# Performance work log

Hardware: AMD Instinct MI355X
Metric: run time of the kernel (lower is better)

Reference implementation:

```python
import jax, jax.numpy as jnp
import numpy as np

N_NODES = 50000
IN_CH = 128
HID = 32
HEADS = 4
OUT_CH = 32
N_EDGES = 1600000
NEG_SLOPE = 0.2


def _gatv2(x, src, dst, Wl, bl, Wr, br, att, bias, H, C):
    """GATv2Conv (PyG semantics, add_self_loops already applied to src/dst).
    x: [N, F_in]; src/dst: [E]; Wl/Wr: [F_in, H*C]; att: [H, C]; bias: [H*C].
    Returns [N, H*C] (concat heads)."""
    N = x.shape[0]
    xl = (x @ Wl + bl).reshape(N, H, C)  # source-side transform
    xr = (x @ Wr + br).reshape(N, H, C)  # target-side transform
    e = jax.nn.leaky_relu(xl[src] + xr[dst], NEG_SLOPE)  # [E, H, C]
    logits = jnp.einsum('ehc,hc->eh', e, att)  # [E, H]
    # softmax over incoming edges of each target node (stable)
    m = jax.ops.segment_max(logits, dst, num_segments=N)[dst]
    p = jnp.exp(logits - m)
    denom = jax.ops.segment_sum(p, dst, num_segments=N)[dst]
    alpha = p / denom  # [E, H]
    out = jax.ops.segment_sum(alpha[:, :, None] * xl[src], dst, num_segments=N)
    return out.reshape(N, H * C) + bias


def setup_inputs() -> dict:
    key = jax.random.key(0)
    ks = jax.random.split(key, 16)
    s1 = 1.0 / np.sqrt(IN_CH)
    s2 = 1.0 / np.sqrt(HID * HEADS)
    inp = {
        'x': jax.random.normal(ks[0], (N_NODES, IN_CH), jnp.float32),
        'edge_index': jax.random.randint(ks[1], (2, N_EDGES), 0, N_NODES, jnp.int64 if jax.config.read('jax_enable_x64') else jnp.int32).astype(jnp.int32),
        # layer 1: in -> HID per head, HEADS heads
        'Wl1': jax.random.normal(ks[2], (IN_CH, HEADS * HID), jnp.float32) * s1,
        'bl1': jnp.zeros((HEADS * HID,), jnp.float32),
        'Wr1': jax.random.normal(ks[3], (IN_CH, HEADS * HID), jnp.float32) * s1,
        'br1': jnp.zeros((HEADS * HID,), jnp.float32),
        'att1': jax.random.normal(ks[4], (HEADS, HID), jnp.float32) * s1,
        'b1': jnp.zeros((HEADS * HID,), jnp.float32),
        # mu head: HID*HEADS -> OUT_CH, 1 head
        'Wl_mu': jax.random.normal(ks[5], (HEADS * HID, OUT_CH), jnp.float32) * s2,
        'bl_mu': jnp.zeros((OUT_CH,), jnp.float32),
        'Wr_mu': jax.random.normal(ks[6], (HEADS * HID, OUT_CH), jnp.float32) * s2,
        'br_mu': jnp.zeros((OUT_CH,), jnp.float32),
        'att_mu': jax.random.normal(ks[7], (1, OUT_CH), jnp.float32) * s2,
        'b_mu': jnp.zeros((OUT_CH,), jnp.float32),
        # logvar head
        'Wl_lv': jax.random.normal(ks[8], (HEADS * HID, OUT_CH), jnp.float32) * s2,
        'bl_lv': jnp.zeros((OUT_CH,), jnp.float32),
        'Wr_lv': jax.random.normal(ks[9], (HEADS * HID, OUT_CH), jnp.float32) * s2,
        'br_lv': jnp.zeros((OUT_CH,), jnp.float32),
        'att_lv': jax.random.normal(ks[10], (1, OUT_CH), jnp.float32) * s2,
        'b_lv': jnp.zeros((OUT_CH,), jnp.float32),
    }
    return inp


def reference(x, edge_index, Wl1, bl1, Wr1, br1, att1, b1,
              Wl_mu, bl_mu, Wr_mu, br_mu, att_mu, b_mu,
              Wl_lv, bl_lv, Wr_lv, br_lv, att_lv, b_lv):
    N = x.shape[0]
    loops = jnp.arange(N, dtype=edge_index.dtype)
    src = jnp.concatenate([edge_index[0], loops])  # add_self_loops=True
    dst = jnp.concatenate([edge_index[1], loops])
    h = jax.nn.relu(_gatv2(x, src, dst, Wl1, bl1, Wr1, br1, att1, b1, HEADS, HID))
    mu = _gatv2(h, src, dst, Wl_mu, bl_mu, Wr_mu, br_mu, att_mu, b_mu, 1, OUT_CH)
    logvar = _gatv2(h, src, dst, Wl_lv, bl_lv, Wr_lv, br_lv, att_lv, b_lv, 1, OUT_CH)
    return (mu, logvar)
```

## Files before the change

kernel.cpp:

```cpp
#include <hip/hip_runtime.h>
#include <hip/hip_fp16.h>

#define NNODES 50000
#define EORIG  1600000
#define ETOT   (EORIG + NNODES)
#define NEG 0.2f
#define BSH 7
#define NBUCK ((NNODES + 127) >> BSH)
#define BCAP 5120
#define NRT (NNODES / 16)
#define EPB 4096
#define LOG2E 1.44269504f

typedef _Float16 v2h __attribute__((ext_vector_type(2)));
typedef _Float16 v8h __attribute__((ext_vector_type(8)));
typedef float    v4f __attribute__((ext_vector_type(4)));

__device__ __forceinline__ float hdot2v(v2h a, v2h b, float c) {
#if __has_builtin(__builtin_amdgcn_fdot2)
    return __builtin_amdgcn_fdot2(a, b, c, false);
#else
    return c + (float)a.x * (float)b.x + (float)a.y * (float)b.y;
#endif
}

__device__ __forceinline__ float fexp2(float t) {
#if __has_builtin(__builtin_amdgcn_exp2f)
    return __builtin_amdgcn_exp2f(t);
#else
    return exp2f(t);
#endif
}

__global__ __launch_bounds__(256) void wcvt_kernel(
    const float* __restrict__ Wl, const float* __restrict__ Wr,
    const float* __restrict__ Wlmu, const float* __restrict__ Wllv,
    const float* __restrict__ Wrmu, const float* __restrict__ Wrlv,
    __half* __restrict__ WT, __half* __restrict__ WT2, int* __restrict__ bcur)
{
    int id = blockIdx.x * 256 + threadIdx.x;
    if (id < NBUCK) bcur[id] = 0;
    if (id < 32768) {
        int k = id >> 8, c = id & 255;
        float v = (c < 128) ? Wl[k * 128 + c] : Wr[k * 128 + (c - 128)];
        WT[c * 128 + k] = __float2half(v);
    } else if (id < 49152) {
        int loc = id - 32768;
        int k = loc >> 7, c = loc & 127;
        int sel = c >> 5, cc = c & 31;
        const float* W = sel == 0 ? Wlmu : sel == 1 ? Wllv : sel == 2 ? Wrmu : Wrlv;
        WT2[c * 128 + k] = __float2half(W[k * 32 + cc]);
    }
}

__global__ __launch_bounds__(256) void lin1_kernel(
    const float* __restrict__ x, const __half* __restrict__ WT,
    const float* __restrict__ bl, const float* __restrict__ br,
    __half* __restrict__ xl16, __half* __restrict__ xr16)
{
    int rt = (blockIdx.x * 256 + threadIdx.x) >> 6;
    if (rt >= NRT) return;
    int l  = threadIdx.x & 63;
    int lr = l & 15, lg = l >> 4;
    int row = rt * 16 + lr;

    v8h a[4];
    const float4* xrow = reinterpret_cast<const float4*>(x + (size_t)row * 128);
    #pragma unroll
    for (int ks = 0; ks < 4; ++ks) {
        float4 f0 = xrow[ks * 8 + lg * 2];
        float4 f1 = xrow[ks * 8 + lg * 2 + 1];
        v8h t;
        t[0]=(_Float16)f0.x; t[1]=(_Float16)f0.y; t[2]=(_Float16)f0.z; t[3]=(_Float16)f0.w;
        t[4]=(_Float16)f1.x; t[5]=(_Float16)f1.y; t[6]=(_Float16)f1.z; t[7]=(_Float16)f1.w;
        a[ks] = t;
    }

    const uint4* wt4 = reinterpret_cast<const uint4*>(WT);
    #pragma unroll 4
    for (int ct = 0; ct < 16; ++ct) {
        int c = ct * 16 + lr;
        v4f acc = {0.f, 0.f, 0.f, 0.f};
        #pragma unroll
        for (int ks = 0; ks < 4; ++ks) {
            union { uint4 u; v8h h; } B;
            B.u = wt4[(size_t)c * 16 + ks * 4 + lg];
            acc = __builtin_amdgcn_mfma_f32_16x16x32_f16(a[ks], B.h, acc, 0, 0, 0);
        }
        float bb = (c < 128) ? bl[c] : br[c - 128];
        #pragma unroll
        for (int j = 0; j < 4; ++j) {
            int orow = rt * 16 + lg * 4 + j;
            __half hv = __float2half(acc[j] + bb);
            if (c < 128) xl16[(size_t)orow * 128 + c] = hv;
            else         xr16[(size_t)orow * 128 + (c - 128)] = hv;
        }
    }
}

__global__ __launch_bounds__(256) void lin2_kernel(
    const __half* __restrict__ h16, const __half* __restrict__ WT2,
    const float* __restrict__ blmu, const float* __restrict__ bllv,
    const float* __restrict__ brmu, const float* __restrict__ brlv,
    __half* __restrict__ xi16, __half* __restrict__ xrI16)
{
    int rt = (blockIdx.x * 256 + threadIdx.x) >> 6;
    if (rt >= NRT) return;
    int l  = threadIdx.x & 63;
    int lr = l & 15, lg = l >> 4;
    int row = rt * 16 + lr;

    v8h a[4];
    const uint4* hrow = reinterpret_cast<const uint4*>(h16 + (size_t)row * 128);
    #pragma unroll
    for (int ks = 0; ks < 4; ++ks) {
        union { uint4 u; v8h h; } A;
        A.u = hrow[ks * 4 + lg];
        a[ks] = A.h;
    }

    const uint4* wt4 = reinterpret_cast<const uint4*>(WT2);
    #pragma unroll 4
    for (int ct = 0; ct < 8; ++ct) {
        int c = ct * 16 + lr;
        v4f acc = {0.f, 0.f, 0.f, 0.f};
        #pragma unroll
        for (int ks = 0; ks < 4; ++ks) {
            union { uint4 u; v8h h; } B;
            B.u = wt4[(size_t)c * 16 + ks * 4 + lg];
            acc = __builtin_amdgcn_mfma_f32_16x16x32_f16(a[ks], B.h, acc, 0, 0, 0);
        }
        int sel = c >> 5, cc = c & 31;
        const float* bp = sel == 0 ? blmu : sel == 1 ? bllv : sel == 2 ? brmu : brlv;
        float bb = bp[cc];
        #pragma unroll
        for (int j = 0; j < 4; ++j) {
            int orow = rt * 16 + lg * 4 + j;
            __half hv = __float2half(acc[j] + bb);
            if (c < 64) xi16 [(size_t)orow * 64 + c]      = hv;
            else        xrI16[(size_t)orow * 64 + (c-64)] = hv;
        }
    }
}

__global__ __launch_bounds__(256) void part_kernel(
    const int* __restrict__ src, const int* __restrict__ dst,
    int* __restrict__ bcur, unsigned int* __restrict__ pairs)
{
    __shared__ int cnt[NBUCK];
    __shared__ int gbase[NBUCK];
    const int e0 = blockIdx.x * EPB;

    for (int i = threadIdx.x; i < NBUCK; i += 256) cnt[i] = 0;
    __syncthreads();

    for (int i = threadIdx.x; i < EPB; i += 256) {
        int e = e0 + i;
        if (e >= ETOT) break;
        int d = (e < EORIG) ? dst[e] : e - EORIG;
        atomicAdd(&cnt[d >> BSH], 1);
    }
    __syncthreads();

    for (int b = threadIdx.x; b < NBUCK; b += 256) {
        int c = cnt[b];
        gbase[b] = c ? (b * BCAP + atomicAdd(&bcur[b], c)) : 0;
        cnt[b] = 0;
    }
    __syncthreads();

    for (int i = threadIdx.x; i < EPB; i += 256) {
        int e = e0 + i;
        if (e >= ETOT) break;
        int s, d;
        if (e < EORIG) { s = src[e]; d = dst[e]; }
        else           { s = d = e - EORIG; }
        int b = d >> BSH;
        int slot = atomicAdd(&cnt[b], 1);
        pairs[gbase[b] + slot] = (unsigned)s | ((unsigned)(d & 127) << 16);
    }
}

__global__ __launch_bounds__(256) void csrfill_kernel(
    const unsigned int* __restrict__ pairs, const int* __restrict__ bcur,
    int2* __restrict__ begend, unsigned short* __restrict__ csr)
{
    __shared__ int cnt[128];
    __shared__ int lofs[128];
    __shared__ int scnt[128];
    const int b = blockIdx.x, n0 = b << BSH;
    const int nn = min(128, NNODES - n0);
    const int pbase = b * BCAP;
    const int pend = pbase + bcur[b];
    const int t = threadIdx.x;

    if (t < 128) { cnt[t] = 0; scnt[t] = 0; }
    __syncthreads();
    for (int i = pbase + t; i < pend; i += 256)
        atomicAdd(&cnt[pairs[i] >> 16], 1);
    __syncthreads();

    if (t < 128) lofs[t] = cnt[t];
    __syncthreads();
    for (int off = 1; off < 128; off <<= 1) {
        int v = (t < 128 && t >= off) ? lofs[t - off] : 0;
        __syncthreads();
        if (t < 128) lofs[t] += v;
        __syncthreads();
    }
    if (t < 128) lofs[t] = pbase + lofs[t] - cnt[t];
    __syncthreads();

    if (t < nn) begend[n0 + t] = make_int2(lofs[t], lofs[t] + cnt[t]);

    for (int i = pbase + t; i < pend; i += 256) {
        unsigned pr = pairs[i];
        int l = pr >> 16;
        int slot = atomicAdd(&scnt[l], 1);
        csr[lofs[l] + slot] = (unsigned short)(pr & 0xFFFFu);
    }
}

__global__ __launch_bounds__(256) void gat_gather1(
    const __half* __restrict__ xl16, const __half* __restrict__ xr16,
    const float* __restrict__ att, const float* __restrict__ bias,
    const int2* __restrict__ begend, const unsigned short* __restrict__ csr,
    __half* __restrict__ h16)
{
    int d = (blockIdx.x * 256 + threadIdx.x) >> 6;
    if (d >= NNODES) return;
    int lane = threadIdx.x & 63;
    int quarter = lane >> 4;
    int q = lane & 15;
    int qo = quarter * 4;

    v2h xrh[4], ath[4];
    {
        union { uint4 u; v2h v[4]; } R;
        R.u = reinterpret_cast<const uint4*>(xr16)[(size_t)d * 16 + q];
        #pragma unroll
        for (int j = 0; j < 4; ++j) xrh[j] = R.v[j];
        const float4* t4 = reinterpret_cast<const float4*>(att) + q * 2;
        float4 a = t4[0], b = t4[1];
        ath[0] = (v2h){(_Float16)(a.x*LOG2E), (_Float16)(a.y*LOG2E)};
        ath[1] = (v2h){(_Float16)(a.z*LOG2E), (_Float16)(a.w*LOG2E)};
        ath[2] = (v2h){(_Float16)(b.x*LOG2E), (_Float16)(b.y*LOG2E)};
        ath[3] = (v2h){(_Float16)(b.z*LOG2E), (_Float16)(b.w*LOG2E)};
    }
    const v2h neg2 = (v2h){(_Float16)NEG, (_Float16)NEG};

    int2 be = begend[d];
    int beg = be.x, end = be.y;
    int nI = (end - beg + 15) >> 4;
    const uint4* xlu = reinterpret_cast<const uint4*>(xl16);

    float den = 0.f;
    float acc[8] = {0.f,0.f,0.f,0.f,0.f,0.f,0.f,0.f};

    auto compute = [&](uint4 U, bool val) {
        union { uint4 u; v2h v[4]; } X; X.u = U;
        float t = 0.f;
        #pragma unroll
        for (int j = 0; j < 4; ++j) {
            v2h s = X.v[j] + xrh[j];
            v2h l = __builtin_elementwise_max(s, s * neg2);
            t = hdot2v(l, ath[j], t);
        }
        t += __shfl_xor(t, 1, 64);
        t += __shfl_xor(t, 2, 64);
        float p = val ? fexp2(t) : 0.f;
        den += p;
        #pragma unroll
        for (int j = 0; j < 4; ++j) {
            acc[2*j]   += p * (float)X.v[j].x;
            acc[2*j+1] += p * (float)X.v[j].y;
        }
    };

    int  iA[4], iB[4];
    bool vA[4], vB[4];
    uint4 rA[4];

    #pragma unroll
    for (int k = 0; k < 4; ++k) {
        int s = beg + qo + k;
        vA[k] = s < end;
        iA[k] = csr[vA[k] ? s : end - 1];
    }
    #pragma unroll
    for (int k = 0; k < 4; ++k) rA[k] = xlu[(size_t)iA[k] * 16 + q];
    #pragma unroll
    for (int k = 0; k < 4; ++k) {
        int s = beg + 16 + qo + k;
        vB[k] = s < end;
        iB[k] = csr[vB[k] ? s : end - 1];
    }

    for (int it = 0; it < nI; ++it) {
        int b2 = beg + (it + 2) * 16;
        int  iC[4]; bool vC[4];
        #pragma unroll
        for (int k = 0; k < 4; ++k) {
            int s = b2 + qo + k;
            vC[k] = s < end;
            iC[k] = csr[vC[k] ? s : end - 1];
        }
        uint4 rB[4];
        #pragma unroll
        for (int k = 0; k < 4; ++k) rB[k] = xlu[(size_t)iB[k] * 16 + q];
        #pragma unroll
        for (int k = 0; k < 4; ++k) compute(rA[k], vA[k]);
        #pragma unroll
        for (int k = 0; k < 4; ++k) {
            rA[k] = rB[k]; vA[k] = vB[k];
            iB[k] = iC[k]; vB[k] = vC[k];
        }
    }

    den += __shfl_xor(den, 16, 64);
    den += __shfl_xor(den, 32, 64);
    #pragma unroll
    for (int j = 0; j < 8; ++j) {
        acc[j] += __shfl_xor(acc[j], 16, 64);
        acc[j] += __shfl_xor(acc[j], 32, 64);
    }

    if (quarter == 0) {
        float r = 1.f / den;
        const float4* bp = reinterpret_cast<const float4*>(bias) + q * 2;
        float4 ba = bp[0], bb = bp[1];
        __half hv[8];
        hv[0] = __float2half(fmaxf(acc[0]*r+ba.x, 0.f));
        hv[1] = __float2half(fmaxf(acc[1]*r+ba.y, 0.f));
        hv[2] = __float2half(fmaxf(acc[2]*r+ba.z, 0.f));
        hv[3] = __float2half(fmaxf(acc[3]*r+ba.w, 0.f));
        hv[4] = __float2half(fmaxf(acc[4]*r+bb.x, 0.f));
        hv[5] = __float2half(fmaxf(acc[5]*r+bb.y, 0.f));
        hv[6] = __float2half(fmaxf(acc[6]*r+bb.z, 0.f));
        hv[7] = __float2half(fmaxf(acc[7]*r+bb.w, 0.f));
        *reinterpret_cast<uint4*>(&h16[(size_t)d * 128 + q * 8]) =
            *reinterpret_cast<uint4*>(hv);
    }
}

__global__ __launch_bounds__(256) void gat_gather2(
    const __half* __restrict__ xi16, const __half* __restrict__ xrI16,
    const float* __restrict__ atmu, const float* __restrict__ atlv,
    const float* __restrict__ bmu,  const float* __restrict__ blv,
    const int2* __restrict__ begend, const unsigned short* __restrict__ csr,
    float* __restrict__ out)
{
    int d = (blockIdx.x * 256 + threadIdx.x) >> 6;
    if (d >= NNODES) return;
    int lane = threadIdx.x & 63;
    int oct = lane >> 3;
    int r   = lane & 7;
    bool lv = r >= 4;
    int cq  = lv ? r - 4 : r;
    int oo = oct * 2;

    v2h xrh[4], ath[4];
    {
        union { uint4 u; v2h v[4]; } R;
        R.u = reinterpret_cast<const uint4*>(xrI16)[(size_t)d * 8 + r];
        #pragma unroll
        for (int j = 0; j < 4; ++j) xrh[j] = R.v[j];
        const float4* t4 = reinterpret_cast<const float4*>(lv ? atlv : atmu) + cq * 2;
        float4 a = t4[0], b = t4[1];
        ath[0] = (v2h){(_Float16)(a.x*LOG2E), (_Float16)(a.y*LOG2E)};
        ath[1] = (v2h){(_Float16)(a.z*LOG2E), (_Float16)(a.w*LOG2E)};
        ath[2] = (v2h){(_Float16)(b.x*LOG2E), (_Float16)(b.y*LOG2E)};
        ath[3] = (v2h){(_Float16)(b.z*LOG2E), (_Float16)(b.w*LOG2E)};
    }
    const v2h neg2 = (v2h){(_Float16)NEG, (_Float16)NEG};

    int2 be = begend[d];
    int beg = be.x, end = be.y;
    int nI = (end - beg + 15) >> 4;
    const uint4* xiu = reinterpret_cast<const uint4*>(xi16);

    float den = 0.f;
    float acc[8] = {0.f,0.f,0.f,0.f,0.f,0.f,0.f,0.f};

    auto compute = [&](uint4 U, bool val) {
        union { uint4 u; v2h v[4]; } X; X.u = U;
        float t = 0.f;
        #pragma unroll
        for (int j = 0; j < 4; ++j) {
            v2h s = X.v[j] + xrh[j];
            v2h l = __builtin_elementwise_max(s, s * neg2);
            t = hdot2v(l, ath[j], t);
        }
        t += __shfl_xor(t, 1, 64);
        t += __shfl_xor(t, 2, 64);
        float p = val ? fexp2(t) : 0.f;
        den += p;
        #pragma unroll
        for (int j = 0; j < 4; ++j) {
            acc[2*j]   += p * (float)X.v[j].x;
            acc[2*j+1] += p * (float)X.v[j].y;
        }
    };

    int  iA[2], iB[2];
    bool vA[2], vB[2];
    uint4 rA[2];

    #pragma unroll
    for (int k = 0; k < 2; ++k) {
        int s = beg + oo + k;
        vA[k] = s < end;
        iA[k] = csr[vA[k] ? s : end - 1];
    }
    #pragma unroll
    for (int k = 0; k < 2; ++k) rA[k] = xiu[(size_t)iA[k] * 8 + r];
    #pragma unroll
    for (int k = 0; k < 2; ++k) {
        int s = beg + 16 + oo + k;
        vB[k] = s < end;
        iB[k] = csr[vB[k] ? s : end - 1];
    }

    for (int it = 0; it < nI; ++it) {
        int b2 = beg + (it + 2) * 16;
        int  iC[2]; bool vC[2];
        #pragma unroll
        for (int k = 0; k < 2; ++k) {
            int s = b2 + oo + k;
            vC[k] = s < end;
            iC[k] = csr[vC[k] ? s : end - 1];
        }
        uint4 rB[2];
        #pragma unroll
        for (int k = 0; k < 2; ++k) rB[k] = xiu[(size_t)iB[k] * 8 + r];
        #pragma unroll
        for (int k = 0; k < 2; ++k) compute(rA[k], vA[k]);
        #pragma unroll
        for (int k = 0; k < 2; ++k) {
            rA[k] = rB[k]; vA[k] = vB[k];
            iB[k] = iC[k]; vB[k] = vC[k];
        }
    }

    den += __shfl_xor(den, 8, 64);
    den += __shfl_xor(den, 16, 64);
    den += __shfl_xor(den, 32, 64);
    #pragma unroll
    for (int j = 0; j < 8; ++j) {
        acc[j] += __shfl_xor(acc[j], 8, 64);
        acc[j] += __shfl_xor(acc[j], 16, 64);
        acc[j] += __shfl_xor(acc[j], 32, 64);
    }

    if (oct == 0) {
        float rr = 1.f / den;
        const float4* bp = reinterpret_cast<const float4*>(lv ? blv : bmu) + cq * 2;
        float4 ba = bp[0], bb = bp[1];
        float4 o1 = make_float4(acc[0]*rr+ba.x, acc[1]*rr+ba.y,
                                acc[2]*rr+ba.z, acc[3]*rr+ba.w);
        float4 o2 = make_float4(acc[4]*rr+bb.x, acc[5]*rr+bb.y,
                                acc[6]*rr+bb.z, acc[7]*rr+bb.w);
        float* base_out = out + (lv ? 1600000 : 0);
        float4* op = reinterpret_cast<float4*>(base_out) + (size_t)d * 8 + cq * 2;
        op[0] = o1; op[1] = o2;
    }
}

extern "C" void kernel_launch(void* const* d_in, const int* in_sizes, int n_in,
                              void* d_out, int out_size, void* d_ws, size_t ws_size,
                              hipStream_t stream) {
    const float* x    = (const float*)d_in[0];
    const int*   ei   = (const int*)d_in[1];
    const float* Wl1  = (const float*)d_in[2];
    const float* bl1  = (const float*)d_in[3];
    const float* Wr1  = (const float*)d_in[4];
    const float* br1  = (const float*)d_in[5];
    const float* att1 = (const float*)d_in[6];
    const float* b1   = (const float*)d_in[7];
    const float* Wlmu = (const float*)d_in[8];
    const float* blmu = (const float*)d_in[9];
    const float* Wrmu = (const float*)d_in[10];
    const float* brmu = (const float*)d_in[11];
    const float* atmu = (const float*)d_in[12];
    const float* bmu  = (const float*)d_in[13];
    const float* Wllv = (const float*)d_in[14];
    const float* bllv = (const float*)d_in[15];
    const float* Wrlv = (const float*)d_in[16];
    const float* brlv = (const float*)d_in[17];
    const float* atlv = (const float*)d_in[18];
    const float* blv  = (const float*)d_in[19];

    float* out = (float*)d_out;
    float* ws  = (float*)d_ws;

    __half* xl16 = (__half*)ws;
    __half* xr16 = (__half*)(ws + 3200000);
    __half* h16  = (__half*)(ws + 6400000);
    __half* WT   = (__half*)(ws + 9600000);
    __half* WT2  = (__half*)(ws + 9620000);

    __half* xi16  = (__half*)ws;
    __half* xrI16 = (__half*)(ws + 1600000);

    int* ip = (int*)(ws + 10000000);
    unsigned int*   pairs  = (unsigned int*)ip;
    int*            bcur   = ip + 2001920;
    int2*           begend = (int2*)(ip + 2002312);
    unsigned short* csr    = (unsigned short*)(ip + 2102312);

    const int* srcp = ei;
    const int* dstp = ei + EORIG;

    const int NBE = (ETOT + EPB - 1) / EPB;

    wcvt_kernel<<<192, 256, 0, stream>>>(Wl1, Wr1, Wlmu, Wllv, Wrmu, Wrlv, WT, WT2, bcur);

    part_kernel<<<NBE, 256, 0, stream>>>(srcp, dstp, bcur, pairs);
    csrfill_kernel<<<NBUCK, 256, 0, stream>>>(pairs, bcur, begend, csr);

    lin1_kernel<<<(NRT + 3) / 4, 256, 0, stream>>>(x, WT, bl1, br1, xl16, xr16);

    gat_gather1<<<(NNODES * 64 + 255) / 256, 256, 0, stream>>>(
        xl16, xr16, att1, b1, begend, csr, h16);

    lin2_kernel<<<(NRT + 3) / 4, 256, 0, stream>>>(
        h16, WT2, blmu, bllv, brmu, brlv, xi16, xrI16);

    gat_gather2<<<(NNODES * 64 + 255) / 256, 256, 0, stream>>>(
        xi16, xrI16, atmu, atlv, bmu, blv, begend, csr, out);
}
```

Before: 198.5 us.

## Store node features head-major and gather one head per wavefront

Node feature buffers move from row-major [N, H*C] to head-major [H, N, 32], and both gather kernels now assign one head of one destination node per wavefront. Eight edges are processed per iteration using 8-byte loads, and blocks are arranged so that wavefronts working on the same head run close together. The goal is a smaller per-head gather footprint, so the source-feature table for that head stays in L2 and the random gathers touch fewer cache lines. The weight conversion is merged into the partition kernel with a memset replacing the in-kernel counter reset. This removes a launch, but the CSR indices and edge lists are now read once per head and each wavefront does less work per load.

```diff
diff --git a/kernel.cpp b/kernel.cpp
--- a/kernel.cpp
+++ b/kernel.cpp
@@ -10,6 +10,7 @@
 #define BCAP 5120
 #define NRT (NNODES / 16)
 #define EPB 4096
+#define NBE ((ETOT + EPB - 1) / EPB)
 #define LOG2E 1.44269504f
 
 typedef _Float16 v2h __attribute__((ext_vector_type(2)));
@@ -32,31 +33,109 @@
 #endif
 }
 
-__global__ __launch_bounds__(256) void wcvt_kernel(
+__global__ __launch_bounds__(256) void prep_kernel(
+    const int* __restrict__ src, const int* __restrict__ dst,
+    int* __restrict__ bcur, unsigned int* __restrict__ pairs,
     const float* __restrict__ Wl, const float* __restrict__ Wr,
     const float* __restrict__ Wlmu, const float* __restrict__ Wllv,
     const float* __restrict__ Wrmu, const float* __restrict__ Wrlv,
-    __half* __restrict__ WT, __half* __restrict__ WT2, int* __restrict__ bcur)
-{
-    int id = blockIdx.x * 256 + threadIdx.x;
-    if (id < NBUCK) bcur[id] = 0;
-    if (id < 32768) {
-        int k = id >> 8, c = id & 255;
-        float v = (c < 128) ? Wl[k * 128 + c] : Wr[k * 128 + (c - 128)];
-        WT[c * 128 + k] = __float2half(v);
-    } else if (id < 49152) {
-        int loc = id - 32768;
-        int k = loc >> 7, c = loc & 127;
-        int sel = c >> 5, cc = c & 31;
-        const float* W = sel == 0 ? Wlmu : sel == 1 ? Wllv : sel == 2 ? Wrmu : Wrlv;
-        WT2[c * 128 + k] = __float2half(W[k * 32 + cc]);
+    __half* __restrict__ WT, __half* __restrict__ WT2)
+{
+    if (blockIdx.x >= NBE) {
+        int id = (blockIdx.x - NBE) * 256 + threadIdx.x;
+        if (id < 32768) {
+            int k = id >> 8, c = id & 255;
+            float v = (c < 128) ? Wl[k * 128 + c] : Wr[k * 128 + (c - 128)];
+            WT[c * 128 + k] = __float2half(v);
+        } else if (id < 49152) {
+            int loc = id - 32768;
+            int k = loc >> 7, c = loc & 127;
+            int sel = c >> 5, cc = c & 31;
+            const float* W = sel == 0 ? Wlmu : sel == 1 ? Wllv : sel == 2 ? Wrmu : Wrlv;
+            WT2[c * 128 + k] = __float2half(W[k * 32 + cc]);
+        }
+        return;
+    }
+
+    __shared__ int cnt[NBUCK];
+    __shared__ int gbase[NBUCK];
+    const int e0 = blockIdx.x * EPB;
+
+    for (int i = threadIdx.x; i < NBUCK; i += 256) cnt[i] = 0;
+    __syncthreads();
+
+    for (int i = threadIdx.x; i < EPB; i += 256) {
+        int e = e0 + i;
+        if (e >= ETOT) break;
+        int d = (e < EORIG) ? dst[e] : e - EORIG;
+        atomicAdd(&cnt[d >> BSH], 1);
+    }
+    __syncthreads();
+
+    for (int b = threadIdx.x; b < NBUCK; b += 256) {
+        int c = cnt[b];
+        gbase[b] = c ? (b * BCAP + atomicAdd(&bcur[b], c)) : 0;
+        cnt[b] = 0;
+    }
+    __syncthreads();
+
+    for (int i = threadIdx.x; i < EPB; i += 256) {
+        int e = e0 + i;
+        if (e >= ETOT) break;
+        int s, d;
+        if (e < EORIG) { s = src[e]; d = dst[e]; }
+        else           { s = d = e - EORIG; }
+        int b = d >> BSH;
+        int slot = atomicAdd(&cnt[b], 1);
+        pairs[gbase[b] + slot] = (unsigned)s | ((unsigned)(d & 127) << 16);
+    }
+}
+
+__global__ __launch_bounds__(256) void csrfill_kernel(
+    const unsigned int* __restrict__ pairs, const int* __restrict__ bcur,
+    int2* __restrict__ begend, unsigned short* __restrict__ csr)
+{
+    __shared__ int cnt[128];
+    __shared__ int lofs[128];
+    __shared__ int scnt[128];
+    const int b = blockIdx.x, n0 = b << BSH;
+    const int nn = min(128, NNODES - n0);
+    const int pbase = b * BCAP;
+    const int pend = pbase + bcur[b];
+    const int t = threadIdx.x;
+
+    if (t < 128) { cnt[t] = 0; scnt[t] = 0; }
+    __syncthreads();
+    for (int i = pbase + t; i < pend; i += 256)
+        atomicAdd(&cnt[pairs[i] >> 16], 1);
+    __syncthreads();
+
+    int myc = (t < 128) ? cnt[t] : 0;
+    if (t < 128) lofs[t] = myc;
+    __syncthreads();
+    for (int off = 1; off < 128; off <<= 1) {
+        int v = (t < 128 && t >= off) ? lofs[t - off] : 0;
+        __syncthreads();
+        if (t < 128) lofs[t] += v;
+        __syncthreads();
+    }
+    if (t < 128) lofs[t] = pbase + lofs[t] - myc;
+    __syncthreads();
+
+    if (t < nn) begend[n0 + t] = make_int2(lofs[t], lofs[t] + myc);
+
+    for (int i = pbase + t; i < pend; i += 256) {
+        unsigned pr = pairs[i];
+        int l = pr >> 16;
+        int slot = atomicAdd(&scnt[l], 1);
+        csr[lofs[l] + slot] = (unsigned short)(pr & 0xFFFFu);
     }
 }
 
 __global__ __launch_bounds__(256) void lin1_kernel(
     const float* __restrict__ x, const __half* __restrict__ WT,
     const float* __restrict__ bl, const float* __restrict__ br,
-    __half* __restrict__ xl16, __half* __restrict__ xr16)
+    __half* __restrict__ xlh, __half* __restrict__ xrh)
 {
     int rt = (blockIdx.x * 256 + threadIdx.x) >> 6;
     if (rt >= NRT) return;
@@ -88,21 +167,22 @@
             acc = __builtin_amdgcn_mfma_f32_16x16x32_f16(a[ks], B.h, acc, 0, 0, 0);
         }
         float bb = (c < 128) ? bl[c] : br[c - 128];
+        int c2 = (c < 128) ? c : c - 128;
+        __half* dstp = (c < 128) ? xlh : xrh;
+        int hh = c2 >> 5, cc = c2 & 31;
         #pragma unroll
         for (int j = 0; j < 4; ++j) {
             int orow = rt * 16 + lg * 4 + j;
-            __half hv = __float2half(acc[j] + bb);
-            if (c < 128) xl16[(size_t)orow * 128 + c] = hv;
-            else         xr16[(size_t)orow * 128 + (c - 128)] = hv;
+            dstp[((size_t)hh * NNODES + orow) * 32 + cc] = __float2half(acc[j] + bb);
         }
     }
 }
 
 __global__ __launch_bounds__(256) void lin2_kernel(
-    const __half* __restrict__ h16, const __half* __restrict__ WT2,
+    const __half* __restrict__ h16h, const __half* __restrict__ WT2,
     const float* __restrict__ blmu, const float* __restrict__ bllv,
     const float* __restrict__ brmu, const float* __restrict__ brlv,
-    __half* __restrict__ xi16, __half* __restrict__ xrI16)
+    __half* __restrict__ xi, __half* __restrict__ xr2)
 {
     int rt = (blockIdx.x * 256 + threadIdx.x) >> 6;
     if (rt >= NRT) return;
@@ -111,11 +191,11 @@
     int row = rt * 16 + lr;
 
     v8h a[4];
-    const uint4* hrow = reinterpret_cast<const uint4*>(h16 + (size_t)row * 128);
     #pragma unroll
     for (int ks = 0; ks < 4; ++ks) {
         union { uint4 u; v8h h; } A;
-        A.u = hrow[ks * 4 + lg];
+        A.u = *reinterpret_cast<const uint4*>(
+            h16h + ((size_t)ks * NNODES + row) * 32 + lg * 8);
         a[ks] = A.h;
     }
 
@@ -133,336 +213,202 @@
         int sel = c >> 5, cc = c & 31;
         const float* bp = sel == 0 ? blmu : sel == 1 ? bllv : sel == 2 ? brmu : brlv;
         float bb = bp[cc];
+        __half* dstp = (sel < 2) ? (xi + (size_t)sel * NNODES * 32)
+                                 : (xr2 + (size_t)(sel - 2) * NNODES * 32);
         #pragma unroll
         for (int j = 0; j < 4; ++j) {
             int orow = rt * 16 + lg * 4 + j;
-            __half hv = __float2half(acc[j] + bb);
-            if (c < 64) xi16 [(size_t)orow * 64 + c]      = hv;
-            else        xrI16[(size_t)orow * 64 + (c-64)] = hv;
+            dstp[(size_t)orow * 32 + cc] = __float2half(acc[j] + bb);
         }
     }
 }
 
-__global__ __launch_bounds__(256) void part_kernel(
-    const int* __restrict__ src, const int* __restrict__ dst,
-    int* __restrict__ bcur, unsigned int* __restrict__ pairs)
-{
-    __shared__ int cnt[NBUCK];
-    __shared__ int gbase[NBUCK];
-    const int e0 = blockIdx.x * EPB;
-
-    for (int i = threadIdx.x; i < NBUCK; i += 256) cnt[i] = 0;
-    __syncthreads();
-
-    for (int i = threadIdx.x; i < EPB; i += 256) {
-        int e = e0 + i;
-        if (e >= ETOT) break;
-        int d = (e < EORIG) ? dst[e] : e - EORIG;
-        atomicAdd(&cnt[d >> BSH], 1);
-    }
-    __syncthreads();
-
-    for (int b = threadIdx.x; b < NBUCK; b += 256) {
-        int c = cnt[b];
-        gbase[b] = c ? (b * BCAP + atomicAdd(&bcur[b], c)) : 0;
-        cnt[b] = 0;
-    }
-    __syncthreads();
-
-    for (int i = threadIdx.x; i < EPB; i += 256) {
-        int e = e0 + i;
-        if (e >= ETOT) break;
-        int s, d;
-        if (e < EORIG) { s = src[e]; d = dst[e]; }
-        else           { s = d = e - EORIG; }
-        int b = d >> BSH;
-        int slot = atomicAdd(&cnt[b], 1);
-        pairs[gbase[b] + slot] = (unsigned)s | ((unsigned)(d & 127) << 16);
-    }
-}
-
-__global__ __launch_bounds__(256) void csrfill_kernel(
-    const unsigned int* __restrict__ pairs, const int* __restrict__ bcur,
-    int2* __restrict__ begend, unsigned short* __restrict__ csr)
-{
-    __shared__ int cnt[128];
-    __shared__ int lofs[128];
-    __shared__ int scnt[128];
-    const int b = blockIdx.x, n0 = b << BSH;
-    const int nn = min(128, NNODES - n0);
-    const int pbase = b * BCAP;
-    const int pend = pbase + bcur[b];
-    const int t = threadIdx.x;
-
-    if (t < 128) { cnt[t] = 0; scnt[t] = 0; }
-    __syncthreads();
-    for (int i = pbase + t; i < pend; i += 256)
-        atomicAdd(&cnt[pairs[i] >> 16], 1);
-    __syncthreads();
-
-    if (t < 128) lofs[t] = cnt[t];
-    __syncthreads();
-    for (int off = 1; off < 128; off <<= 1) {
-        int v = (t < 128 && t >= off) ? lofs[t - off] : 0;
-        __syncthreads();
-        if (t < 128) lofs[t] += v;
-        __syncthreads();
-    }
-    if (t < 128) lofs[t] = pbase + lofs[t] - cnt[t];
-    __syncthreads();
-
-    if (t < nn) begend[n0 + t] = make_int2(lofs[t], lofs[t] + cnt[t]);
-
-    for (int i = pbase + t; i < pend; i += 256) {
-        unsigned pr = pairs[i];
-        int l = pr >> 16;
-        int slot = atomicAdd(&scnt[l], 1);
-        csr[lofs[l] + slot] = (unsigned short)(pr & 0xFFFFu);
-    }
-}
-
 __global__ __launch_bounds__(256) void gat_gather1(
-    const __half* __restrict__ xl16, const __half* __restrict__ xr16,
+    const __half* __restrict__ xlh, const __half* __restrict__ xrh,
     const float* __restrict__ att, const float* __restrict__ bias,
     const int2* __restrict__ begend, const unsigned short* __restrict__ csr,
-    __half* __restrict__ h16)
-{
-    int d = (blockIdx.x * 256 + threadIdx.x) >> 6;
+    __half* __restrict__ h16h)
+{
+    int b = blockIdx.x;
+    int s = b & 7;
+    int head = s >> 1;
+    int d = (b >> 3) * 8 + (s & 1) * 4 + (threadIdx.x >> 6);
     if (d >= NNODES) return;
     int lane = threadIdx.x & 63;
-    int quarter = lane >> 4;
-    int q = lane & 15;
-    int qo = quarter * 4;
-
-    v2h xrh[4], ath[4];
+    int g = lane >> 3;
+    int c = lane & 7;
+
+    v2h xrv[2], atv[2];
     {
-        union { uint4 u; v2h v[4]; } R;
-        R.u = reinterpret_cast<const uint4*>(xr16)[(size_t)d * 16 + q];
-        #pragma unroll
-        for (int j = 0; j < 4; ++j) xrh[j] = R.v[j];
-        const float4* t4 = reinterpret_cast<const float4*>(att) + q * 2;
-        float4 a = t4[0], b = t4[1];
-        ath[0] = (v2h){(_Float16)(a.x*LOG2E), (_Float16)(a.y*LOG2E)};
-        ath[1] = (v2h){(_Float16)(a.z*LOG2E), (_Float16)(a.w*LOG2E)};
-        ath[2] = (v2h){(_Float16)(b.x*LOG2E), (_Float16)(b.y*LOG2E)};
-        ath[3] = (v2h){(_Float16)(b.z*LOG2E), (_Float16)(b.w*LOG2E)};
+        union { uint2 u; v2h v[2]; } R;
+        R.u = reinterpret_cast<const uint2*>(xrh + ((size_t)head * NNODES + d) * 32)[c];
+        xrv[0] = R.v[0]; xrv[1] = R.v[1];
+        float4 a = reinterpret_cast<const float4*>(att + head * 32)[c];
+        atv[0] = (v2h){(_Float16)(a.x*LOG2E), (_Float16)(a.y*LOG2E)};
+        atv[1] = (v2h){(_Float16)(a.z*LOG2E), (_Float16)(a.w*LOG2E)};
     }
     const v2h neg2 = (v2h){(_Float16)NEG, (_Float16)NEG};
 
     int2 be = begend[d];
     int beg = be.x, end = be.y;
-    int nI = (end - beg + 15) >> 4;
-    const uint4* xlu = reinterpret_cast<const uint4*>(xl16);
+    int nI = (end - beg + 7) >> 3;
+    const uint2* xlu = reinterpret_cast<const uint2*>(xlh + (size_t)head * NNODES * 32);
 
     float den = 0.f;
-    float acc[8] = {0.f,0.f,0.f,0.f,0.f,0.f,0.f,0.f};
-
-    auto compute = [&](uint4 U, bool val) {
-        union { uint4 u; v2h v[4]; } X; X.u = U;
-        float t = 0.f;
-        #pragma unroll
-        for (int j = 0; j < 4; ++j) {
-            v2h s = X.v[j] + xrh[j];
-            v2h l = __builtin_elementwise_max(s, s * neg2);
-            t = hdot2v(l, ath[j], t);
-        }
+    float acc[4] = {0.f, 0.f, 0.f, 0.f};
+
+    auto compute = [&](uint2 U, bool val) {
+        union { uint2 u; v2h v[2]; } X; X.u = U;
+        v2h s0 = X.v[0] + xrv[0];
+        v2h s1 = X.v[1] + xrv[1];
+        v2h l0 = __builtin_elementwise_max(s0, s0 * neg2);
+        v2h l1 = __builtin_elementwise_max(s1, s1 * neg2);
+        float t = hdot2v(l0, atv[0], 0.f);
+        t = hdot2v(l1, atv[1], t);
         t += __shfl_xor(t, 1, 64);
         t += __shfl_xor(t, 2, 64);
+        t += __shfl_xor(t, 4, 64);
         float p = val ? fexp2(t) : 0.f;
         den += p;
-        #pragma unroll
-        for (int j = 0; j < 4; ++j) {
-            acc[2*j]   += p * (float)X.v[j].x;
-            acc[2*j+1] += p * (float)X.v[j].y;
-        }
+        acc[0] += p * (float)X.v[0].x;
+        acc[1] += p * (float)X.v[0].y;
+        acc[2] += p * (float)X.v[1].x;
+        acc[3] += p * (float)X.v[1].y;
     };
 
-    int  iA[4], iB[4];
-    bool vA[4], vB[4];
-    uint4 rA[4];
-
-    #pragma unroll
-    for (int k = 0; k < 4; ++k) {
-        int s = beg + qo + k;
-        vA[k] = s < end;
-        iA[k] = csr[vA[k] ? s : end - 1];
-    }
-    #pragma unroll
-    for (int k = 0; k < 4; ++k) rA[k] = xlu[(size_t)iA[k] * 16 + q];
-    #pragma unroll
-    for (int k = 0; k < 4; ++k) {
-        int s = beg + 16 + qo + k;
-        vB[k] = s < end;
-        iB[k] = csr[vB[k] ? s : end - 1];
-    }
+    int sA = beg + g;
+    bool vA = sA < end;
+    int iA = csr[vA ? sA : end - 1];
+    uint2 rA = xlu[(size_t)iA * 8 + c];
+    int sB = beg + 8 + g;
+    bool vB = sB < end;
+    int iB = csr[vB ? sB : end - 1];
 
     for (int it = 0; it < nI; ++it) {
-        int b2 = beg + (it + 2) * 16;
-        int  iC[4]; bool vC[4];
-        #pragma unroll
-        for (int k = 0; k < 4; ++k) {
-            int s = b2 + qo + k;
-            vC[k] = s < end;
-            iC[k] = csr[vC[k] ? s : end - 1];
-        }
-        uint4 rB[4];
-        #pragma unroll
-        for (int k = 0; k < 4; ++k) rB[k] = xlu[(size_t)iB[k] * 16 + q];
-        #pragma unroll
-        for (int k = 0; k < 4; ++k) compute(rA[k], vA[k]);
-        #pragma unroll
-        for (int k = 0; k < 4; ++k) {
-            rA[k] = rB[k]; vA[k] = vB[k];
-            iB[k] = iC[k]; vB[k] = vC[k];
-        }
-    }
-
+        int sC = beg + (it + 2) * 8 + g;
+        bool vC = sC < end;
+        int iC = csr[vC ? sC : end - 1];
+        uint2 rB = xlu[(size_t)iB * 8 + c];
+        compute(rA, vA);
+        rA = rB; vA = vB; iB = iC; vB = vC;
+    }
+
+    den += __shfl_xor(den, 8, 64);
     den += __shfl_xor(den, 16, 64);
     den += __shfl_xor(den, 32, 64);
     #pragma unroll
-    for (int j = 0; j < 8; ++j) {
+    for (int j = 0; j < 4; ++j) {
+        acc[j] += __shfl_xor(acc[j], 8, 64);
         acc[j] += __shfl_xor(acc[j], 16, 64);
         acc[j] += __shfl_xor(acc[j], 32, 64);
     }
 
-    if (quarter == 0) {
+    if (g == 0) {
         float r = 1.f / den;
-        const float4* bp = reinterpret_cast<const float4*>(bias) + q * 2;
-        float4 ba = bp[0], bb = bp[1];
-        __half hv[8];
-        hv[0] = __float2half(fmaxf(acc[0]*r+ba.x, 0.f));
-        hv[1] = __float2half(fmaxf(acc[1]*r+ba.y, 0.f));
-        hv[2] = __float2half(fmaxf(acc[2]*r+ba.z, 0.f));
-        hv[3] = __float2half(fmaxf(acc[3]*r+ba.w, 0.f));
-        hv[4] = __float2half(fmaxf(acc[4]*r+bb.x, 0.f));
-        hv[5] = __float2half(fmaxf(acc[5]*r+bb.y, 0.f));
-        hv[6] = __float2half(fmaxf(acc[6]*r+bb.z, 0.f));
-        hv[7] = __float2half(fmaxf(acc[7]*r+bb.w, 0.f));
-        *reinterpret_cast<uint4*>(&h16[(size_t)d * 128 + q * 8]) =
-            *reinterpret_cast<uint4*>(hv);
+        float4 bb = reinterpret_cast<const float4*>(bias + head * 32)[c];
+        __half hv[4];
+        hv[0] = __float2half(fmaxf(acc[0] * r + bb.x, 0.f));
+        hv[1] = __float2half(fmaxf(acc[1] * r + bb.y, 0.f));
+        hv[2] = __float2half(fmaxf(acc[2] * r + bb.z, 0.f));
+        hv[3] = __float2half(fmaxf(acc[3] * r + bb.w, 0.f));
+        *reinterpret_cast<uint2*>(&h16h[((size_t)head * NNODES + d) * 32 + c * 4]) =
+            *reinterpret_cast<uint2*>(hv);
     }
 }
 
 __global__ __launch_bounds__(256) void gat_gather2(
-    const __half* __restrict__ xi16, const __half* __restrict__ xrI16,
+    const __half* __restrict__ xi, const __half* __restrict__ xr2,
     const float* __restrict__ atmu, const float* __restrict__ atlv,
     const float* __restrict__ bmu,  const float* __restrict__ blv,
     const int2* __restrict__ begend, const unsigned short* __restrict__ csr,
     float* __restrict__ out)
 {
-    int d = (blockIdx.x * 256 + threadIdx.x) >> 6;
+    int b = blockIdx.x;
+    int s = b & 7;
+    int head = s >> 2;
+    int d = (b >> 3) * 16 + (s & 3) * 4 + (threadIdx.x >> 6);
     if (d >= NNODES) return;
     int lane = threadIdx.x & 63;
-    int oct = lane >> 3;
-    int r   = lane & 7;
-    bool lv = r >= 4;
-    int cq  = lv ? r - 4 : r;
-    int oo = oct * 2;
-
-    v2h xrh[4], ath[4];
+    int g = lane >> 3;
+    int c = lane & 7;
+
+    const __half* xip  = xi  + (size_t)head * NNODES * 32;
+    const __half* xrp  = xr2 + (size_t)head * NNODES * 32;
+    const float*  atp  = head ? atlv : atmu;
+    const float*  bp   = head ? blv : bmu;
+
+    v2h xrv[2], atv[2];
     {
-        union { uint4 u; v2h v[4]; } R;
-        R.u = reinterpret_cast<const uint4*>(xrI16)[(size_t)d * 8 + r];
-        #pragma unroll
-        for (int j = 0; j < 4; ++j) xrh[j] = R.v[j];
-        const float4* t4 = reinterpret_cast<const float4*>(lv ? atlv : atmu) + cq * 2;
-        float4 a = t4[0], b = t4[1];
-        ath[0] = (v2h){(_Float16)(a.x*LOG2E), (_Float16)(a.y*LOG2E)};
-        ath[1] = (v2h){(_Float16)(a.z*LOG2E), (_Float16)(a.w*LOG2E)};
-        ath[2] = (v2h){(_Float16)(b.x*LOG2E), (_Float16)(b.y*LOG2E)};
-        ath[3] = (v2h){(_Float16)(b.z*LOG2E), (_Float16)(b.w*LOG2E)};
+        union { uint2 u; v2h v[2]; } R;
+        R.u = reinterpret_cast<const uint2*>(xrp + (size_t)d * 32)[c];
+        xrv[0] = R.v[0]; xrv[1] = R.v[1];
+        float4 a = reinterpret_cast<const float4*>(atp)[c];
+        atv[0] = (v2h){(_Float16)(a.x*LOG2E), (_Float16)(a.y*LOG2E)};
+        atv[1] = (v2h){(_Float16)(a.z*LOG2E), (_Float16)(a.w*LOG2E)};
     }
     const v2h neg2 = (v2h){(_Float16)NEG, (_Float16)NEG};
 
     int2 be = begend[d];
     int beg = be.x, end = be.y;
-    int nI = (end - beg + 15) >> 4;
-    const uint4* xiu = reinterpret_cast<const uint4*>(xi16);
+    int nI = (end - beg + 7) >> 3;
+    const uint2* xiu = reinterpret_cast<const uint2*>(xip);
 
     float den = 0.f;
-    float acc[8] = {0.f,0.f,0.f,0.f,0.f,0.f,0.f,0.f};
-
-    auto compute = [&](uint4 U, bool val) {
-        union { uint4 u; v2h v[4]; } X; X.u = U;
-        float t = 0.f;
-        #pragma unroll
-        for (int j = 0; j < 4; ++j) {
-            v2h s = X.v[j] + xrh[j];
-            v2h l = __builtin_elementwise_max(s, s * neg2);
-            t = hdot2v(l, ath[j], t);
-        }
+    float acc[4] = {0.f, 0.f, 0.f, 0.f};
+
+    auto compute = [&](uint2 U, bool val) {
+        union { uint2 u; v2h v[2]; } X; X.u = U;
+        v2h s0 = X.v[0] + xrv[0];
+        v2h s1 = X.v[1] + xrv[1];
+        v2h l0 = __builtin_elementwise_max(s0, s0 * neg2);
+        v2h l1 = __builtin_elementwise_max(s1, s1 * neg2);
+        float t = hdot2v(l0, atv[0], 0.f);
+        t = hdot2v(l1, atv[1], t);
         t += __shfl_xor(t, 1, 64);
         t += __shfl_xor(t, 2, 64);
+        t += __shfl_xor(t, 4, 64);
         float p = val ? fexp2(t) : 0.f;
         den += p;
-        #pragma unroll
-        for (int j = 0; j < 4; ++j) {
-            acc[2*j]   += p * (float)X.v[j].x;
-            acc[2*j+1] += p * (float)X.v[j].y;
-        }
+        acc[0] += p * (float)X.v[0].x;
+        acc[1] += p * (float)X.v[0].y;
+        acc[2] += p * (float)X.v[1].x;
+        acc[3] += p * (float)X.v[1].y;
     };
 
-    int  iA[2], iB[2];
-    bool vA[2], vB[2];
-    uint4 rA[2];
-
-    #pragma unroll
-    for (int k = 0; k < 2; ++k) {
-        int s = beg + oo + k;
-        vA[k] = s < end;
-        iA[k] = csr[vA[k] ? s : end - 1];
-    }
-    #pragma unroll
-    for (int k = 0; k < 2; ++k) rA[k] = xiu[(size_t)iA[k] * 8 + r];
-    #pragma unroll
-    for (int k = 0; k < 2; ++k) {
-        int s = beg + 16 + oo + k;
-        vB[k] = s < end;
-        iB[k] = csr[vB[k] ? s : end - 1];
-    }
+    int sA = beg + g;
+    bool vA = sA < end;
+    int iA = csr[vA ? sA : end - 1];
+    uint2 rA = xiu[(size_t)iA * 8 + c];
+    int sB = beg + 8 + g;
+    bool vB = sB < end;
+    int iB = csr[vB ? sB : end - 1];
 
     for (int it = 0; it < nI; ++it) {
-        int b2 = beg + (it + 2) * 16;
-        int  iC[2]; bool vC[2];
-        #pragma unroll
-        for (int k = 0; k < 2; ++k) {
-            int s = b2 + oo + k;
-            vC[k] = s < end;
-            iC[k] = csr[vC[k] ? s : end - 1];
-        }
-        uint4 rB[2];
-        #pragma unroll
-        for (int k = 0; k < 2; ++k) rB[k] = xiu[(size_t)iB[k] * 8 + r];
-        #pragma unroll
-        for (int k = 0; k < 2; ++k) compute(rA[k], vA[k]);
-        #pragma unroll
-        for (int k = 0; k < 2; ++k) {
-            rA[k] = rB[k]; vA[k] = vB[k];
-            iB[k] = iC[k]; vB[k] = vC[k];
-        }
+        int sC = beg + (it + 2) * 8 + g;
+        bool vC = sC < end;
+        int iC = csr[vC ? sC : end - 1];
+        uint2 rB = xiu[(size_t)iB * 8 + c];
+        compute(rA, vA);
+        rA = rB; vA = vB; iB = iC; vB = vC;
     }
 
     den += __shfl_xor(den, 8, 64);
     den += __shfl_xor(den, 16, 64);
     den += __shfl_xor(den, 32, 64);
     #pragma unroll
-    for (int j = 0; j < 8; ++j) {
+    for (int j = 0; j < 4; ++j) {
         acc[j] += __shfl_xor(acc[j], 8, 64);
         acc[j] += __shfl_xor(acc[j], 16, 64);
         acc[j] += __shfl_xor(acc[j], 32, 64);
     }
 
-    if (oct == 0) {
-        float rr = 1.f / den;
-        const float4* bp = reinterpret_cast<const float4*>(lv ? blv : bmu) + cq * 2;
-        float4 ba = bp[0], bb = bp[1];
-        float4 o1 = make_float4(acc[0]*rr+ba.x, acc[1]*rr+ba.y,
-                                acc[2]*rr+ba.z, acc[3]*rr+ba.w);
-        float4 o2 = make_float4(acc[4]*rr+bb.x, acc[5]*rr+bb.y,
-                                acc[6]*rr+bb.z, acc[7]*rr+bb.w);
-        float* base_out = out + (lv ? 1600000 : 0);
-        float4* op = reinterpret_cast<float4*>(base_out) + (size_t)d * 8 + cq * 2;
-        op[0] = o1; op[1] = o2;
+    if (g == 0) {
+        float r = 1.f / den;
+        float4 bb = reinterpret_cast<const float4*>(bp)[c];
+        float4 o = make_float4(acc[0]*r+bb.x, acc[1]*r+bb.y,
+                               acc[2]*r+bb.z, acc[3]*r+bb.w);
+        float* base_out = out + (head ? 1600000 : 0);
+        reinterpret_cast<float4*>(base_out + (size_t)d * 32)[c] = o;
     }
 }
 
@@ -493,14 +439,14 @@
     float* out = (float*)d_out;
     float* ws  = (float*)d_ws;
 
-    __half* xl16 = (__half*)ws;
-    __half* xr16 = (__half*)(ws + 3200000);
-    __half* h16  = (__half*)(ws + 6400000);
+    __half* xlh  = (__half*)ws;
+    __half* xrh  = (__half*)(ws + 3200000);
+    __half* h16h = (__half*)(ws + 6400000);
     __half* WT   = (__half*)(ws + 9600000);
     __half* WT2  = (__half*)(ws + 9620000);
 
-    __half* xi16  = (__half*)ws;
-    __half* xrI16 = (__half*)(ws + 1600000);
+    __half* xi  = (__half*)ws;
+    __half* xr2 = (__half*)(ws + 1600000);
 
     int* ip = (int*)(ws + 10000000);
     unsigned int*   pairs  = (unsigned int*)ip;
@@ -511,21 +457,19 @@
     const int* srcp = ei;
     const int* dstp = ei + EORIG;
 
-    const int NBE = (ETOT + EPB - 1) / EPB;
-
-    wcvt_kernel<<<192, 256, 0, stream>>>(Wl1, Wr1, Wlmu, Wllv, Wrmu, Wrlv, WT, WT2, bcur);
-
-    part_kernel<<<NBE, 256, 0, stream>>>(srcp, dstp, bcur, pairs);
+    hipMemsetAsync(bcur, 0, NBUCK * sizeof(int), stream);
+    prep_kernel<<<NBE + 192, 256, 0, stream>>>(
+        srcp, dstp, bcur, pairs, Wl1, Wr1, Wlmu, Wllv, Wrmu, Wrlv, WT, WT2);
     csrfill_kernel<<<NBUCK, 256, 0, stream>>>(pairs, bcur, begend, csr);
 
-    lin1_kernel<<<(NRT + 3) / 4, 256, 0, stream>>>(x, WT, bl1, br1, xl16, xr16);
-
-    gat_gather1<<<(NNODES * 64 + 255) / 256, 256, 0, stream>>>(
-        xl16, xr16, att1, b1, begend, csr, h16);
+    lin1_kernel<<<(NRT + 3) / 4, 256, 0, stream>>>(x, WT, bl1, br1, xlh, xrh);
+
+    gat_gather1<<<(NNODES / 8) * 8, 256, 0, stream>>>(
+        xlh, xrh, att1, b1, begend, csr, h16h);
 
     lin2_kernel<<<(NRT + 3) / 4, 256, 0, stream>>>(
-        h16, WT2, blmu, bllv, brmu, brlv, xi16, xrI16);
-
-    gat_gather2<<<(NNODES * 64 + 255) / 256, 256, 0, stream>>>(
-        xi16, xrI16, atmu, atlv, bmu, blv, begend, csr, out);
-}
+        h16h, WT2, blmu, bllv, brmu, brlv, xi, xr2);
+
+    gat_gather2<<<(NNODES / 16) * 8, 256, 0, stream>>>(
+        xi, xr2, atmu, atlv, bmu, blv, begend, csr, out);
+}
```

After: 259.4 us. 30.7% more time.
